# Kernel tuning notes

Hardware: AMD Instinct MI355X
Metric: run time of the kernel (lower is better)

Reference implementation:

```python
import jax, jax.numpy as jnp
import numpy as np

B, L, D, H, F = 4, 2048, 768, 12, 3072
ROUTE_FRAC = 0.15
LN_EPS = 1e-5


def _ln(x, g, b):
    m = jnp.mean(x, axis=-1, keepdims=True)
    v = jnp.mean((x - m) ** 2, axis=-1, keepdims=True)
    return (x - m) * jax.lax.rsqrt(v + LN_EPS) * g + b


def setup_inputs() -> dict:
    key = jax.random.key(0)
    ks = jax.random.split(key, 20)
    s = 0.02
    return {
        "hidden_states": jax.random.normal(ks[0], (B, L, D), dtype=jnp.float32),
        "g1": jnp.ones((D,), jnp.float32), "b1": jnp.zeros((D,), jnp.float32),
        "g2": jnp.ones((D,), jnp.float32), "b2": jnp.zeros((D,), jnp.float32),
        "Wr": jax.random.normal(ks[1], (D,), jnp.float32) * s, "br": jnp.zeros((), jnp.float32),
        "Wq": jax.random.normal(ks[2], (D, D), jnp.float32) * s, "bq": jnp.zeros((D,), jnp.float32),
        "Wk": jax.random.normal(ks[3], (D, D), jnp.float32) * s, "bk": jnp.zeros((D,), jnp.float32),
        "Wv": jax.random.normal(ks[4], (D, D), jnp.float32) * s, "bv": jnp.zeros((D,), jnp.float32),
        "Wo": jax.random.normal(ks[5], (D, D), jnp.float32) * s, "bo": jnp.zeros((D,), jnp.float32),
        "Wm": jax.random.normal(ks[6], (D, D), jnp.float32) * s, "bm": jnp.zeros((D,), jnp.float32),
        "W1": jax.random.normal(ks[7], (D, F), jnp.float32) * s, "bf1": jnp.zeros((F,), jnp.float32),
        "W2": jax.random.normal(ks[8], (F, D), jnp.float32) * s, "bf2": jnp.zeros((D,), jnp.float32),
    }


def reference(hidden_states, g1, b1, g2, b2, Wr, br, Wq, bq, Wk, bk, Wv, bv, Wo, bo, Wm, bm, W1, bf1, W2, bf2):
    b, l, d = hidden_states.shape
    dh = d // H
    normed = _ln(hidden_states, g1, b1)  # [B,L,D]

    # Router: per-token coherence score; lowest-coherence route_frac tokens get attention.
    scores = jax.nn.sigmoid(jnp.einsum('bld,d->bl', normed, Wr) + br)  # [B,L]
    k = max(1, int(round(ROUTE_FRAC * l)))
    _, idx = jax.lax.top_k(-scores, k)  # lowest-coherence token indices
    attn_mask = jnp.zeros((b, l), bool).at[jnp.arange(b)[:, None], idx].set(True)

    # Attention path (computed densely over all tokens, as the torch module does).
    q = (normed @ Wq + bq).reshape(b, l, H, dh)
    kk = (normed @ Wk + bk).reshape(b, l, H, dh)
    v = (normed @ Wv + bv).reshape(b, l, H, dh)
    logits = jnp.einsum('blhd,bmhd->bhlm', q, kk) / jnp.sqrt(jnp.float32(dh))
    probs = jax.nn.softmax(logits, axis=-1)
    ctx = jnp.einsum('bhlm,bmhd->blhd', probs, v).reshape(b, l, d)
    attn_out = ctx @ Wo + bo

    # Lightweight coherence-mixing path: coherence-weighted global pooling + linear.
    w = scores / (jnp.sum(scores, axis=1, keepdims=True) + 1e-6)
    pooled = jnp.einsum('bl,bld->bd', w, normed)  # [B,D]
    mix_out = (normed + scores[..., None] * pooled[:, None, :]) @ Wm + bm

    merged = jnp.where(attn_mask[..., None], attn_out, mix_out)
    h = hidden_states + merged  # dropout is identity at eval

    n2 = _ln(h, g2, b2)
    ffn = jax.nn.gelu(n2 @ W1 + bf1, approximate=False) @ W2 + bf2
    return h + ffn
```

## Files before the change

kernel.cpp:

```cpp
#include <hip/hip_runtime.h>
#include <math.h>

#define B_ 4
#define L_ 2048
#define D_ 768
#define H_ 12
#define F_ 3072
#define KTOP 307
#define KPAD 320
#define LN_EPS 1e-5f

typedef unsigned int u32;
typedef unsigned short u16;
using bf16x8 = __attribute__((ext_vector_type(8))) short;
using f32x4  = __attribute__((ext_vector_type(4))) float;

#define AS1 __attribute__((address_space(1)))
#define AS3 __attribute__((address_space(3)))

__device__ __forceinline__ void gl16(const void* g, void* l) {
    __builtin_amdgcn_global_load_lds((const AS1 u32*)g, (AS3 u32*)l, 16, 0, 0);
}
__device__ __forceinline__ void wait_vm0() {
    asm volatile("s_waitcnt vmcnt(0)" ::: "memory");
}
__device__ __forceinline__ u16 f2bf(float f) {
    u32 u = __float_as_uint(f);
    return (u16)((u + 0x7fff + ((u >> 16) & 1)) >> 16);
}
__device__ __forceinline__ float bf2f(u16 s) {
    return __uint_as_float(((u32)s) << 16);
}
__device__ __forceinline__ float gelu_tanh(float v) {
    float u = v * v * v;
    float z = fmaf(u, 0.0713548163f, 1.59576912f * v);
    float s = __builtin_amdgcn_rcpf(1.0f + __expf(-z));
    return v * s;
}

__device__ __forceinline__ float blk_reduce_sum(float v, float* red) {
    #pragma unroll
    for (int off = 32; off; off >>= 1) v += __shfl_xor(v, off, 64);
    __syncthreads();
    if ((threadIdx.x & 63) == 0) red[threadIdx.x >> 6] = v;
    __syncthreads();
    return red[0] + red[1] + red[2] + red[3];
}
__device__ __forceinline__ void blk_reduce_sum2(
    float a, float b, float* red, float& oa, float& ob)
{
    #pragma unroll
    for (int off = 32; off; off >>= 1) {
        a += __shfl_xor(a, off, 64);
        b += __shfl_xor(b, off, 64);
    }
    __syncthreads();
    if ((threadIdx.x & 63) == 0) {
        int w = threadIdx.x >> 6;
        red[w] = a; red[4 + w] = b;
    }
    __syncthreads();
    oa = red[0] + red[1] + red[2] + red[3];
    ob = red[4] + red[5] + red[6] + red[7];
}

template <bool SCORE>
__global__ __launch_bounds__(256) void ln_kernel(
    const float* __restrict__ x, const float* __restrict__ g,
    const float* __restrict__ be, const float* __restrict__ Wr,
    const float* __restrict__ brp, u16* __restrict__ outn,
    float* __restrict__ scores)
{
    __shared__ float red[8];
    const int t = blockIdx.x;
    const int tid = threadIdx.x;
    const float* xr = x + (size_t)t * D_;
    float v0 = xr[tid], v1 = xr[tid + 256], v2 = xr[tid + 512];
    float s1, s2;
    blk_reduce_sum2(v0 + v1 + v2,
                    fmaf(v0, v0, fmaf(v1, v1, v2 * v2)), red, s1, s2);
    float mean = s1 * (1.0f / 768.0f);
    float var  = fmaf(-mean, mean, s2 * (1.0f / 768.0f));
    float inv = 1.0f / sqrtf(fmaxf(var, 0.f) + LN_EPS);
    float n0 = (v0 - mean) * inv * g[tid] + be[tid];
    float n1 = (v1 - mean) * inv * g[tid + 256] + be[tid + 256];
    float n2 = (v2 - mean) * inv * g[tid + 512] + be[tid + 512];
    u16* orow = outn + (size_t)t * D_;
    orow[tid] = f2bf(n0); orow[tid + 256] = f2bf(n1); orow[tid + 512] = f2bf(n2);
    if (SCORE) {
        __syncthreads();
        float dot = blk_reduce_sum(n0 * Wr[tid] + n1 * Wr[tid + 256] + n2 * Wr[tid + 512], red);
        if (tid == 0) scores[t] = 1.0f / (1.0f + expf(-(dot + brp[0])));
    }
}

__global__ __launch_bounds__(1024) void topk_kernel(
    const float* __restrict__ scores, unsigned* __restrict__ mask,
    float* __restrict__ ssum, int* __restrict__ rowmap, int* __restrict__ inv)
{
    __shared__ u32 sb[L_];
    __shared__ u32 hist[256];
    __shared__ u32 wsum[16];
    __shared__ float redf[16];
    __shared__ u32 bcast[2];
    __shared__ u32 cnt_sel;
    const int b = blockIdx.x, tid = threadIdx.x;
    const int lane = tid & 63, wv = tid >> 6;

    if (tid == 0) cnt_sel = 0;
    float s0 = scores[b * L_ + tid];
    float s1 = scores[b * L_ + tid + 1024];
    sb[tid] = __float_as_uint(s0);
    sb[tid + 1024] = __float_as_uint(s1);
    float v = s0 + s1;
    #pragma unroll
    for (int o = 32; o; o >>= 1) v += __shfl_xor(v, o, 64);
    if (lane == 0) redf[wv] = v;
    __syncthreads();
    if (tid == 0) {
        float t = 0.f;
        #pragma unroll
        for (int w = 0; w < 16; w++) t += redf[w];
        ssum[b] = t;
    }

    u32 want = KTOP, prefix = 0;
    #pragma unroll
    for (int pass = 0; pass < 4; pass++) {
        const int shift = 24 - pass * 8;
        if (tid < 256) hist[tid] = 0;
        __syncthreads();
        u32 x0 = sb[tid], x1 = sb[tid + 1024];
        if (pass == 0 || (x0 >> (shift + 8)) == prefix) atomicAdd(&hist[(x0 >> shift) & 255], 1u);
        if (pass == 0 || (x1 >> (shift + 8)) == prefix) atomicAdd(&hist[(x1 >> shift) & 255], 1u);
        __syncthreads();
        u32 c = 0, inc = 0;
        if (tid < 256) {
            c = hist[tid];
            inc = c;
            #pragma unroll
            for (int o = 1; o < 64; o <<= 1) {
                u32 t = __shfl_up(inc, o, 64);
                if (lane >= o) inc += t;
            }
            if (lane == 63) wsum[wv] = inc;
        }
        __syncthreads();
        if (tid < 256) {
            u32 base = 0;
            #pragma unroll
            for (int w = 0; w < 4; w++) if (w < wv) base += wsum[w];
            u32 incl = base + inc;
            u32 excl = incl - c;
            if (excl < want && want <= incl) {
                bcast[0] = (u32)tid;
                bcast[1] = want - excl;
            }
        }
        __syncthreads();
        prefix = (prefix << 8) | bcast[0];
        want = bcast[1];
    }

    const u32 sstar = prefix;
    u32 a0 = sb[2 * tid], a1 = sb[2 * tid + 1];
    u32 e0 = (a0 == sstar) ? 1u : 0u, e1 = (a1 == sstar) ? 1u : 0u;
    u32 ps = e0 + e1, inc2 = ps;
    #pragma unroll
    for (int o = 1; o < 64; o <<= 1) {
        u32 t = __shfl_up(inc2, o, 64);
        if (lane >= o) inc2 += t;
    }
    __syncthreads();
    if (lane == 63) wsum[wv] = inc2;
    __syncthreads();
    u32 base = 0;
    #pragma unroll
    for (int w = 0; w < 16; w++) if (w < wv) base += wsum[w];
    u32 excl0 = base + inc2 - ps;
    {
        int i = 2 * tid;
        bool sel = (a0 < sstar) || (e0 && (excl0 < want));
        mask[b * L_ + i] = sel ? 1u : 0u;
        int invv = 0;
        if (sel) {
            u32 slot = atomicAdd(&cnt_sel, 1u);
            rowmap[b * KPAD + slot] = b * L_ + i;
            invv = b * KPAD + (int)slot;
        }
        inv[b * L_ + i] = invv;
    }
    {
        int i = 2 * tid + 1;
        u32 r1 = excl0 + e0;
        bool sel = (a1 < sstar) || (e1 && (r1 < want));
        mask[b * L_ + i] = sel ? 1u : 0u;
        int invv = 0;
        if (sel) {
            u32 slot = atomicAdd(&cnt_sel, 1u);
            rowmap[b * KPAD + slot] = b * L_ + i;
            invv = b * KPAD + (int)slot;
        }
        inv[b * L_ + i] = invv;
    }
    if (tid < KPAD - KTOP)
        rowmap[b * KPAD + KTOP + tid] = b * L_;
}

__global__ __launch_bounds__(256) void pooled_part(
    const float* __restrict__ scores, const u16* __restrict__ nb,
    float* __restrict__ parts)
{
    const int lc = blockIdx.x, b = blockIdx.y, tid = threadIdx.x;
    float a0 = 0.f, a1 = 0.f, a2 = 0.f;
    const int l0 = lc * 32;
    for (int l = l0; l < l0 + 32; l++) {
        float s = scores[b * L_ + l];
        const u16* row = nb + (size_t)(b * L_ + l) * D_;
        a0 += s * bf2f(row[tid]);
        a1 += s * bf2f(row[tid + 256]);
        a2 += s * bf2f(row[tid + 512]);
    }
    float* p = parts + (size_t)(lc * B_ + b) * D_;
    p[tid] = a0; p[tid + 256] = a1; p[tid + 512] = a2;
}

__global__ __launch_bounds__(256) void pooled_wm(
    const float* __restrict__ parts, const float* __restrict__ ssum,
    const float* __restrict__ Wm, float* __restrict__ pWm)
{
    __shared__ float pl[768];
    __shared__ float red2[4][64];
    const int b = blockIdx.y, n0 = blockIdx.x * 64, tid = threadIdx.x;
    float inv = 1.0f / (ssum[b] + 1e-6f);
    for (int d = tid; d < 768; d += 256) {
        float s = 0.f;
        #pragma unroll 8
        for (int lc = 0; lc < 64; lc++) s += parts[(size_t)(lc * B_ + b) * D_ + d];
        pl[d] = s * inv;
    }
    __syncthreads();
    const int nl = tid & 63, kq = tid >> 6;
    const int n = n0 + nl;
    float acc = 0.f;
    const int k0 = kq * 192;
    for (int k = k0; k < k0 + 192; k++)
        acc = fmaf(pl[k], Wm[(size_t)k * D_ + n], acc);
    red2[kq][nl] = acc;
    __syncthreads();
    if (kq == 0)
        pWm[b * D_ + n] = red2[0][nl] + red2[1][nl] + red2[2][nl] + red2[3][nl];
}

__global__ __launch_bounds__(256) void wconv_all(
    const float* __restrict__ Wq, const float* __restrict__ Wk,
    const float* __restrict__ Wv, const float* __restrict__ Wo,
    const float* __restrict__ Wm, const float* __restrict__ W1,
    const float* __restrict__ W2,
    u16* __restrict__ WqT, u16* __restrict__ WkvT, u16* __restrict__ WoT,
    u16* __restrict__ WmT, u16* __restrict__ W1T, u16* __restrict__ W2T,
    const float* __restrict__ bq, const float* __restrict__ bk,
    const float* __restrict__ bv, float* __restrict__ bqs,
    float* __restrict__ bkv)
{
    __shared__ float t[32][33];
    int id = blockIdx.x;
    const int tid = threadIdx.x;
    if (id >= 7488) {
        for (int i = tid; i < 768; i += 256) {
            bqs[i] = bq[i] * 0.125f;
            bkv[i] = bk[i];
            bkv[768 + i] = bv[i];
        }
        return;
    }
    const float* src; u16* dst; int K, N, local; float sc = 1.f;
    if (id < 576)       { src = Wq; dst = WqT; K = 768; N = 768; local = id; sc = 0.125f; }
    else if (id < 1152) { src = Wk; dst = WkvT;            K = 768; N = 768; local = id - 576; }
    else if (id < 1728) { src = Wv; dst = WkvT + 768 * 768; K = 768; N = 768; local = id - 1152; }
    else if (id < 2304) { src = Wo; dst = WoT; K = 768; N = 768; local = id - 1728; }
    else if (id < 2880) { src = Wm; dst = WmT; K = 768; N = 768; local = id - 2304; }
    else if (id < 5184) { src = W1; dst = W1T; K = 768; N = 3072; local = id - 2880; }
    else                { src = W2; dst = W2T; K = 3072; N = 768; local = id - 5184; }
    const int ntiles = N >> 5;
    const int n0 = (local % ntiles) * 32, k0 = (local / ntiles) * 32;
    const int tx = tid & 31, ty = tid >> 5;
    #pragma unroll
    for (int i = 0; i < 4; i++)
        t[ty + i * 8][tx] = src[(size_t)(k0 + ty + i * 8) * N + n0 + tx];
    __syncthreads();
    #pragma unroll
    for (int i = 0; i < 4; i++)
        dst[(size_t)(n0 + ty + i * 8) * K + k0 + tx] = f2bf(t[tx][ty + i * 8] * sc);
}

template <int EPI, bool RMAP, int TM>
__global__ __launch_bounds__(256) void mfma_gemm(
    const u16* __restrict__ A, const u16* __restrict__ Bt,
    const float* __restrict__ bias, void* __restrict__ Cout,
    int N, int K, int nbn,
    const float* __restrict__ x, const unsigned* __restrict__ msk,
    const float* __restrict__ attn, const float* __restrict__ scores,
    const float* __restrict__ pWm, const float* __restrict__ hres,
    const int* __restrict__ rowmap, const int* __restrict__ invmap)
{
    constexpr int NI = (TM == 128) ? 4 : 2;
    constexpr int ASLOTS = TM * 8 / 256;
    __shared__ u16 Asm[2][TM * 64];
    __shared__ u16 Bsm[2][128 * 64];
    const int tid = threadIdx.x;
    const int wave = tid >> 6, lane = tid & 63;
    const int quad = lane >> 4, l15 = lane & 15;

    const int nwg = gridDim.x;
    const int bid = blockIdx.x;
    const int wid = ((nwg & 7) == 0) ? ((bid & 7) * (nwg >> 3) + (bid >> 3)) : bid;
    const int m0 = (wid / nbn) * TM, n0 = (wid % nbn) * 128;
    const int wm = (TM == 128) ? (wave >> 1) * 64 : 0;
    const int wn = (TM == 128) ? (wave & 1) * 64 : wave * 32;

    f32x4 acc[4][NI];
    #pragma unroll
    for (int i = 0; i < 4; i++)
        #pragma unroll
        for (int j = 0; j < NI; j++) acc[i][j] = 0.f;

    const u16* ap[ASLOTS]; const u16* bp[4];
    #pragma unroll
    for (int i = 0; i < ASLOTS; i++) {
        int s = i * 256 + tid;
        int row = s >> 3;
        int kq = (s & 7) ^ (row & 7);
        int arow = RMAP ? rowmap[m0 + row] : (m0 + row);
        ap[i] = A + (size_t)arow * K + kq * 8;
    }
    #pragma unroll
    for (int i = 0; i < 4; i++) {
        int s = i * 256 + tid;
        int row = s >> 3;
        int kq = (s & 7) ^ (row & 7);
        bp[i] = Bt + (size_t)(n0 + row) * K + kq * 8;
    }

    auto stage = [&](int buf) {
        #pragma unroll
        for (int i = 0; i < ASLOTS; i++) {
            gl16(ap[i], &Asm[buf][(i * 256 + wave * 64) * 8]);
            ap[i] += 64;
        }
        #pragma unroll
        for (int i = 0; i < 4; i++) {
            gl16(bp[i], &Bsm[buf][(i * 256 + wave * 64) * 8]);
            bp[i] += 64;
        }
    };
    auto compute = [&](int buf) {
        #pragma unroll
        for (int kk = 0; kk < 2; kk++) {
            bf16x8 af[4], bfr[NI];
            const int kq = kk * 4 + quad;
            #pragma unroll
            for (int mi = 0; mi < 4; mi++) {
                int row = wm + mi * 16 + l15;
                af[mi] = *(const bf16x8*)&Asm[buf][(row * 8 + (kq ^ (row & 7))) * 8];
            }
            #pragma unroll
            for (int ni = 0; ni < NI; ni++) {
                int row = wn + ni * 16 + l15;
                bfr[ni] = *(const bf16x8*)&Bsm[buf][(row * 8 + (kq ^ (row & 7))) * 8];
            }
            #pragma unroll
            for (int mi = 0; mi < 4; mi++)
                #pragma unroll
                for (int ni = 0; ni < NI; ni++)
                    acc[mi][ni] = __builtin_amdgcn_mfma_f32_16x16x32_bf16(
                        af[mi], bfr[ni], acc[mi][ni], 0, 0, 0);
        }
    };

    const int nt = K >> 6;
    stage(0);
    wait_vm0();
    __syncthreads();
    for (int t = 0; t < nt; t += 2) {
        stage(1);
        compute(0);
        wait_vm0();
        __syncthreads();
        if (t + 2 < nt) stage(0);
        compute(1);
        if (t + 2 < nt) {
            wait_vm0();
            __syncthreads();
        }
    }

    #pragma unroll
    for (int mi = 0; mi < 4; mi++) {
        #pragma unroll
        for (int ni = 0; ni < NI; ni++) {
            #pragma unroll
            for (int r = 0; r < 4; r++) {
                int row = m0 + wm + mi * 16 + quad * 4 + r;
                int col = n0 + wn + ni * 16 + l15;
                float v = acc[mi][ni][r] + bias[col];
                size_t off = (size_t)row * N + col;
                if (EPI == 0) ((float*)Cout)[off] = v;
                else if (EPI == 1) ((u16*)Cout)[off] = f2bf(v);
                else if (EPI == 2) ((u16*)Cout)[off] = f2bf(gelu_tanh(v));
                else if (EPI == 3) {
                    float mix = v + scores[row] * pWm[(row >> 11) * D_ + col];
                    float sel = msk[row] ? attn[(size_t)invmap[row] * D_ + col] : mix;
                    ((float*)Cout)[off] = x[off] + sel;
                } else {
                    ((float*)Cout)[off] = v + hres[off];
                }
            }
        }
    }
}

__global__ __launch_bounds__(256) void vtrans(
    const u16* __restrict__ V, u16* __restrict__ VT, int ld)
{
    __shared__ u16 tl[64 * 72];
    const int tid = threadIdx.x;
    const int l0 = blockIdx.x * 64, h = blockIdx.y, b = blockIdx.z;
    const u16* src = V + h * 64;
    {
        int r = tid >> 3, ch = tid & 7;
        *(uint4*)&tl[r * 72 + ch * 8] =
            *(const uint4*)&src[(size_t)(b * L_ + l0 + r) * ld + ch * 8];
        int t2 = tid + 256; r = t2 >> 3; ch = t2 & 7;
        *(uint4*)&tl[r * 72 + ch * 8] =
            *(const uint4*)&src[(size_t)(b * L_ + l0 + r) * ld + ch * 8];
    }
    __syncthreads();
    int d = tid >> 2, lg = (tid & 3) * 16;
    u16* dst = VT + (size_t)((b * H_ + h) * 64 + d) * L_ + l0 + lg;
    union { u16 s[8]; uint4 v; } pk;
    #pragma unroll
    for (int j = 0; j < 8; j++) pk.s[j] = tl[(lg + j) * 72 + d];
    *(uint4*)dst = pk.v;
    #pragma unroll
    for (int j = 0; j < 8; j++) pk.s[j] = tl[(lg + 8 + j) * 72 + d];
    *(uint4*)(dst + 8) = pk.v;
}

__global__ __launch_bounds__(256) void attn2(
    const u16* __restrict__ qcomp, const u16* __restrict__ Kg,
    const u16* __restrict__ VTg, u16* __restrict__ ctxc)
{
    __shared__ u16 Qs[64 * 64];
    __shared__ u16 Ks[2][64 * 64];
    __shared__ u16 Vs[2][64 * 64];
    __shared__ u16 Ps[4 * 16 * 72];
    const int tid = threadIdx.x, wave = tid >> 6, lane = tid & 63;
    const int quad = lane >> 4, l15 = lane & 15;
    const int qb = blockIdx.x, h = blockIdx.y, b = blockIdx.z;
    const int q0 = qb * 64;

    {
        int s0 = wave * 64 + lane;
        int r = s0 >> 3, c = (s0 & 7) ^ (r & 7);
        gl16(qcomp + (size_t)(b * KPAD + q0 + r) * D_ + h * 64 + c * 8,
             &Qs[(wave * 64) * 8]);
        int s1 = s0 + 256;
        int r1 = s1 >> 3, c1 = (s1 & 7) ^ (r1 & 7);
        gl16(qcomp + (size_t)(b * KPAD + q0 + r1) * D_ + h * 64 + c1 * 8,
             &Qs[(256 + wave * 64) * 8]);
    }
    const u16 *kp0, *kp1, *vp0, *vp1;
    {
        int s0 = wave * 64 + lane;
        int r = s0 >> 3, c = (s0 & 7) ^ (r & 7);
        kp0 = Kg + (size_t)(b * L_ + r) * 1536 + h * 64 + c * 8;
        vp0 = VTg + (size_t)((b * H_ + h) * 64 + r) * L_ + c * 8;
        int s1 = s0 + 256;
        int r1 = s1 >> 3, c1 = (s1 & 7) ^ (r1 & 7);
        kp1 = Kg + (size_t)(b * L_ + r1) * 1536 + h * 64 + c1 * 8;
        vp1 = VTg + (size_t)((b * H_ + h) * 64 + r1) * L_ + c1 * 8;
    }
    gl16(kp0, &Ks[0][(wave * 64) * 8]);        kp0 += (size_t)64 * 1536;
    gl16(kp1, &Ks[0][(256 + wave * 64) * 8]);  kp1 += (size_t)64 * 1536;
    gl16(vp0, &Vs[0][(wave * 64) * 8]);        vp0 += 64;
    gl16(vp1, &Vs[0][(256 + wave * 64) * 8]);  vp1 += 64;
    wait_vm0();
    __syncthreads();
    bf16x8 qf0, qf1;
    {
        int row = wave * 16 + l15;
        qf0 = *(const bf16x8*)&Qs[(row * 8 + ((quad)     ^ (row & 7))) * 8];
        qf1 = *(const bf16x8*)&Qs[(row * 8 + ((4 + quad) ^ (row & 7))) * 8];
    }
    f32x4 accO[4]; float lp[4];
    #pragma unroll
    for (int i = 0; i < 4; i++) { accO[i] = 0.f; lp[i] = 0.f; }
    u16* Psw = Ps + wave * 16 * 72;

    for (int kt = 0; kt < L_; kt += 64) {
        const int buf = (kt >> 6) & 1;
        if (kt + 64 < L_) {
            gl16(kp0, &Ks[buf ^ 1][(wave * 64) * 8]);        kp0 += (size_t)64 * 1536;
            gl16(kp1, &Ks[buf ^ 1][(256 + wave * 64) * 8]);  kp1 += (size_t)64 * 1536;
            gl16(vp0, &Vs[buf ^ 1][(wave * 64) * 8]);        vp0 += 64;
            gl16(vp1, &Vs[buf ^ 1][(256 + wave * 64) * 8]);  vp1 += 64;
        }

        f32x4 accS[4];
        #pragma unroll
        for (int ni = 0; ni < 4; ni++) accS[ni] = 0.f;
        #pragma unroll
        for (int kk = 0; kk < 2; kk++) {
            const int kq = kk * 4 + quad;
            #pragma unroll
            for (int ni = 0; ni < 4; ni++) {
                int row = ni * 16 + l15;
                bf16x8 kf = *(const bf16x8*)&Ks[buf][(row * 8 + (kq ^ (row & 7))) * 8];
                accS[ni] = __builtin_amdgcn_mfma_f32_16x16x32_bf16(
                    kk ? qf1 : qf0, kf, accS[ni], 0, 0, 0);
            }
        }
        #pragma unroll
        for (int ni = 0; ni < 4; ni++) {
            #pragma unroll
            for (int r = 0; r < 4; r++) {
                float p = __expf(accS[ni][r]);
                lp[r] += p;
                Psw[(quad * 4 + r) * 72 + ni * 16 + l15] = f2bf(p);
            }
        }
        #pragma unroll
        for (int kk = 0; kk < 2; kk++) {
            bf16x8 pf = *(const bf16x8*)&Psw[l15 * 72 + kk * 32 + quad * 8];
            const int kq = kk * 4 + quad;
            #pragma unroll
            for (int ni = 0; ni < 4; ni++) {
                int row = ni * 16 + l15;
                bf16x8 vf = *(const bf16x8*)&Vs[buf][(row * 8 + (kq ^ (row & 7))) * 8];
                accO[ni] = __builtin_amdgcn_mfma_f32_16x16x32_bf16(pf, vf, accO[ni], 0, 0, 0);
            }
        }
        wait_vm0();
        __syncthreads();
    }

    float invl[4];
    #pragma unroll
    for (int r = 0; r < 4; r++) {
        float s = lp[r];
        s += __shfl_xor(s, 1, 64); s += __shfl_xor(s, 2, 64);
        s += __shfl_xor(s, 4, 64); s += __shfl_xor(s, 8, 64);
        invl[r] = 1.0f / s;
    }
    #pragma unroll
    for (int ni = 0; ni < 4; ni++) {
        #pragma unroll
        for (int r = 0; r < 4; r++) {
            int ql = q0 + wave * 16 + quad * 4 + r;
            if (ql < KTOP)
                ctxc[(size_t)(b * KPAD + ql) * D_ + h * 64 + ni * 16 + l15] =
                    f2bf(accO[ni][r] * invl[r]);
        }
    }
}

extern "C" void kernel_launch(void* const* d_in, const int* in_sizes, int n_in,
                              void* d_out, int out_size, void* d_ws, size_t ws_size,
                              hipStream_t stream)
{
    const float* x   = (const float*)d_in[0];
    const float* g1  = (const float*)d_in[1];
    const float* b1  = (const float*)d_in[2];
    const float* g2  = (const float*)d_in[3];
    const float* b2  = (const float*)d_in[4];
    const float* Wr  = (const float*)d_in[5];
    const float* br  = (const float*)d_in[6];
    const float* Wq  = (const float*)d_in[7];
    const float* bq  = (const float*)d_in[8];
    const float* Wk  = (const float*)d_in[9];
    const float* bk  = (const float*)d_in[10];
    const float* Wv  = (const float*)d_in[11];
    const float* bv  = (const float*)d_in[12];
    const float* Wo  = (const float*)d_in[13];
    const float* bo  = (const float*)d_in[14];
    const float* Wm  = (const float*)d_in[15];
    const float* bm  = (const float*)d_in[16];
    const float* W1  = (const float*)d_in[17];
    const float* bf1 = (const float*)d_in[18];
    const float* W2  = (const float*)d_in[19];
    const float* bf2 = (const float*)d_in[20];
    float* out = (float*)d_out;

    char* W = (char*)d_ws;
    u16* WqT  = (u16*)(W + 0);
    u16* WkvT = (u16*)(W + 1179648);
    u16* WoT  = (u16*)(W + 3538944);
    u16* WmT  = (u16*)(W + 4718592);
    u16* W1T  = (u16*)(W + 5898240);
    u16* W2T  = (u16*)(W + 10616832);
    float* scores  = (float*)(W + 15335424);
    unsigned* mask = (unsigned*)(W + 15368192);
    float* ssum    = (float*)(W + 15400960);
    float* pWm     = (float*)(W + 15413504);
    float* bkv     = (float*)(W + 15524096);
    float* bqs     = (float*)(W + 15530240);
    int* rowmap    = (int*)(W + 15533312);
    int* invmap    = (int*)(W + 15538432);
    u16* nb    = (u16*)(W + 15728640);
    u16* Y     = (u16*)(W + 28311552);
    u16* qcomp = (u16*)(W + 53477376);
    u16* ctxc  = (u16*)(W + 55443456);
    float* attnc = (float*)(W + 57409536);
    u16* VT    = (u16*)(W + 61341696);
    float* h   = (float*)(W + 28311552);
    u16* n2b   = (u16*)(W + 15728640);
    u16* mid   = (u16*)(W + 53477376);
    float* parts = (float*)(W + 53477376);

    wconv_all<<<7489, 256, 0, stream>>>(Wq, Wk, Wv, Wo, Wm, W1, W2,
                                        WqT, WkvT, WoT, WmT, W1T, W2T,
                                        bq, bk, bv, bqs, bkv);

    const int NT = B_ * L_;
    ln_kernel<true><<<NT, 256, 0, stream>>>(x, g1, b1, Wr, br, nb, scores);
    topk_kernel<<<B_, 1024, 0, stream>>>(scores, mask, ssum, rowmap, invmap);
    pooled_part<<<dim3(64, B_), 256, 0, stream>>>(scores, nb, parts);
    pooled_wm<<<dim3(12, B_), 256, 0, stream>>>(parts, ssum, Wm, pWm);

    mfma_gemm<1, false, 128><<<768, 256, 0, stream>>>(nb, WkvT, bkv, Y, 1536, 768, 12,
        nullptr, nullptr, nullptr, nullptr, nullptr, nullptr, nullptr, nullptr);
    mfma_gemm<1, true, 64><<<120, 256, 0, stream>>>(nb, WqT, bqs, qcomp, 768, 768, 6,
        nullptr, nullptr, nullptr, nullptr, nullptr, nullptr, rowmap, nullptr);
    vtrans<<<dim3(32, H_, B_), 256, 0, stream>>>(Y + 768, VT, 1536);
    attn2<<<dim3(KPAD / 64, H_, B_), 256, 0, stream>>>(qcomp, Y, VT, ctxc);
    mfma_gemm<0, false, 64><<<120, 256, 0, stream>>>(ctxc, WoT, bo, attnc, 768, 768, 6,
        nullptr, nullptr, nullptr, nullptr, nullptr, nullptr, nullptr, nullptr);
    mfma_gemm<3, false, 64><<<768, 256, 0, stream>>>(nb, WmT, bm, h, 768, 768, 6,
        x, mask, attnc, scores, pWm, nullptr, nullptr, invmap);
    ln_kernel<false><<<NT, 256, 0, stream>>>(h, g2, b2, nullptr, nullptr, n2b, nullptr);
    mfma_gemm<2, false, 128><<<1536, 256, 0, stream>>>(n2b, W1T, bf1, mid, 3072, 768, 24,
        nullptr, nullptr, nullptr, nullptr, nullptr, nullptr, nullptr, nullptr);
    mfma_gemm<4, false, 64><<<768, 256, 0, stream>>>(mid, W2T, bf2, out, 768, 3072, 6,
        nullptr, nullptr, nullptr, nullptr, nullptr, h, nullptr, nullptr);
}
```

Measured before the change: 419.9 us.

## Deepen GEMM pipeline to four-stage K=32 ring with partial vmcnt waits

Restructures the MFMA GEMM main loop from a double-buffered K=64 scheme with full vmcnt(0) waits into a 4-slot ring of K=32 tiles, keeping three loads in flight. Each iteration waits only for the oldest stage using a counted s_waitcnt and a single barrier. The goal is to hide global-to-LDS latency better and drop the second barrier per step. In exchange there are twice as many iterations and barriers per K, and correctness depends on the hand-tuned vmcnt counts matching the number of loads issued per stage.

```diff
diff --git a/kernel.cpp b/kernel.cpp
--- a/kernel.cpp
+++ b/kernel.cpp
@@ -305,9 +305,9 @@
     const int* __restrict__ rowmap, const int* __restrict__ invmap)
 {
     constexpr int NI = (TM == 128) ? 4 : 2;
-    constexpr int ASLOTS = TM * 8 / 256;
-    __shared__ u16 Asm[2][TM * 64];
-    __shared__ u16 Bsm[2][128 * 64];
+    constexpr int AL = TM / 64;
+    __shared__ u16 Asm[4][TM * 32];
+    __shared__ u16 Bsm[4][128 * 32];
     const int tid = threadIdx.x;
     const int wave = tid >> 6, lane = tid & 63;
     const int quad = lane >> 4, l15 = lane & 15;
@@ -325,74 +325,70 @@
         #pragma unroll
         for (int j = 0; j < NI; j++) acc[i][j] = 0.f;
 
-    const u16* ap[ASLOTS]; const u16* bp[4];
-    #pragma unroll
-    for (int i = 0; i < ASLOTS; i++) {
+    const u16* ap[AL]; const u16* bp[2];
+    #pragma unroll
+    for (int i = 0; i < AL; i++) {
         int s = i * 256 + tid;
-        int row = s >> 3;
-        int kq = (s & 7) ^ (row & 7);
+        int row = s >> 2;
+        int cs = (s & 3) ^ (row & 3);
         int arow = RMAP ? rowmap[m0 + row] : (m0 + row);
-        ap[i] = A + (size_t)arow * K + kq * 8;
-    }
-    #pragma unroll
-    for (int i = 0; i < 4; i++) {
+        ap[i] = A + (size_t)arow * K + cs * 8;
+    }
+    #pragma unroll
+    for (int i = 0; i < 2; i++) {
         int s = i * 256 + tid;
-        int row = s >> 3;
-        int kq = (s & 7) ^ (row & 7);
-        bp[i] = Bt + (size_t)(n0 + row) * K + kq * 8;
+        int row = s >> 2;
+        int cs = (s & 3) ^ (row & 3);
+        bp[i] = Bt + (size_t)(n0 + row) * K + cs * 8;
     }
 
     auto stage = [&](int buf) {
         #pragma unroll
-        for (int i = 0; i < ASLOTS; i++) {
+        for (int i = 0; i < AL; i++) {
             gl16(ap[i], &Asm[buf][(i * 256 + wave * 64) * 8]);
-            ap[i] += 64;
-        }
-        #pragma unroll
-        for (int i = 0; i < 4; i++) {
+            ap[i] += 32;
+        }
+        #pragma unroll
+        for (int i = 0; i < 2; i++) {
             gl16(bp[i], &Bsm[buf][(i * 256 + wave * 64) * 8]);
-            bp[i] += 64;
+            bp[i] += 32;
         }
     };
     auto compute = [&](int buf) {
-        #pragma unroll
-        for (int kk = 0; kk < 2; kk++) {
-            bf16x8 af[4], bfr[NI];
-            const int kq = kk * 4 + quad;
+        bf16x8 af[4], bfr[NI];
+        #pragma unroll
+        for (int mi = 0; mi < 4; mi++) {
+            int row = wm + mi * 16 + l15;
+            af[mi] = *(const bf16x8*)&Asm[buf][(row * 4 + (quad ^ (row & 3))) * 8];
+        }
+        #pragma unroll
+        for (int ni = 0; ni < NI; ni++) {
+            int row = wn + ni * 16 + l15;
+            bfr[ni] = *(const bf16x8*)&Bsm[buf][(row * 4 + (quad ^ (row & 3))) * 8];
+        }
+        #pragma unroll
+        for (int mi = 0; mi < 4; mi++)
             #pragma unroll
-            for (int mi = 0; mi < 4; mi++) {
-                int row = wm + mi * 16 + l15;
-                af[mi] = *(const bf16x8*)&Asm[buf][(row * 8 + (kq ^ (row & 7))) * 8];
-            }
-            #pragma unroll
-            for (int ni = 0; ni < NI; ni++) {
-                int row = wn + ni * 16 + l15;
-                bfr[ni] = *(const bf16x8*)&Bsm[buf][(row * 8 + (kq ^ (row & 7))) * 8];
-            }
-            #pragma unroll
-            for (int mi = 0; mi < 4; mi++)
-                #pragma unroll
-                for (int ni = 0; ni < NI; ni++)
-                    acc[mi][ni] = __builtin_amdgcn_mfma_f32_16x16x32_bf16(
-                        af[mi], bfr[ni], acc[mi][ni], 0, 0, 0);
-        }
+            for (int ni = 0; ni < NI; ni++)
+                acc[mi][ni] = __builtin_amdgcn_mfma_f32_16x16x32_bf16(
+                    af[mi], bfr[ni], acc[mi][ni], 0, 0, 0);
     };
 
-    const int nt = K >> 6;
-    stage(0);
-    wait_vm0();
-    __syncthreads();
-    for (int t = 0; t < nt; t += 2) {
-        stage(1);
-        compute(0);
-        wait_vm0();
-        __syncthreads();
-        if (t + 2 < nt) stage(0);
-        compute(1);
-        if (t + 2 < nt) {
-            wait_vm0();
-            __syncthreads();
-        }
+    const int nt = K >> 5;
+    stage(0); stage(1); stage(2);
+    for (int t = 0; t < nt; t++) {
+        if (t < nt - 2) {
+            if constexpr (TM == 128) asm volatile("s_waitcnt vmcnt(8)" ::: "memory");
+            else                     asm volatile("s_waitcnt vmcnt(6)" ::: "memory");
+        } else if (t == nt - 2) {
+            if constexpr (TM == 128) asm volatile("s_waitcnt vmcnt(4)" ::: "memory");
+            else                     asm volatile("s_waitcnt vmcnt(3)" ::: "memory");
+        } else {
+            asm volatile("s_waitcnt vmcnt(0)" ::: "memory");
+        }
+        __builtin_amdgcn_s_barrier();
+        if (t + 3 < nt) stage((t + 3) & 3);
+        compute(t & 3);
     }
 
     #pragma unroll
```

After: 464.4 us. +10.6%, slower.
